# Performance work log

Measured on AMD Instinct MI355X. Metric: run time of the kernel, lower is better.

Reference implementation:

```python
import jax, jax.numpy as jnp
import numpy as np

N_NODES = 100000
N_EDGES = 1600000
IN_CH = 128
HID = 64
BN_EPS = 1e-5


def setup_inputs() -> dict:
    key = jax.random.key(0)
    ks = jax.random.split(key, 16)
    x = jax.random.normal(ks[0], (N_NODES, IN_CH), dtype=jnp.float32)
    edge_index = jax.random.randint(ks[1], (2, N_EDGES), 0, N_NODES, dtype=jnp.int32)
    edge_weight = jax.random.uniform(ks[2], (N_EDGES,), dtype=jnp.float32)
    # GCNConv layer params (weight [in, out], bias [out])
    W1 = jax.random.normal(ks[3], (IN_CH, HID), dtype=jnp.float32) / np.sqrt(IN_CH)
    b1 = jnp.zeros((HID,), jnp.float32)
    W2 = jax.random.normal(ks[4], (HID, HID), dtype=jnp.float32) / np.sqrt(HID)
    b2 = jnp.zeros((HID,), jnp.float32)
    # BatchNorm affine params
    g1 = jnp.ones((HID,), jnp.float32)
    beta1 = jnp.zeros((HID,), jnp.float32)
    g2 = jnp.ones((HID,), jnp.float32)
    beta2 = jnp.zeros((HID,), jnp.float32)
    # input projection for residual (in_channels != hidden_dim)
    pW = jax.random.normal(ks[5], (IN_CH, HID), dtype=jnp.float32) / np.sqrt(IN_CH)
    pb = jnp.zeros((HID,), jnp.float32)
    return {"x": x, "edge_index": edge_index, "edge_weight": edge_weight,
            "W1": W1, "b1": b1, "g1": g1, "beta1": beta1,
            "W2": W2, "b2": b2, "g2": g2, "beta2": beta2,
            "pW": pW, "pb": pb}


def _gcn_norm(edge_index, edge_weight, num_nodes):
    # add self-loops with weight 1, symmetric normalization (PyG gcn_norm)
    loop = jnp.arange(num_nodes, dtype=edge_index.dtype)
    row = jnp.concatenate([edge_index[0], loop])   # source
    col = jnp.concatenate([edge_index[1], loop])   # target
    w = jnp.concatenate([edge_weight, jnp.ones((num_nodes,), edge_weight.dtype)])
    deg = jax.ops.segment_sum(w, col, num_segments=num_nodes)  # weighted in-degree
    dis = jnp.where(deg > 0, jax.lax.rsqrt(jnp.where(deg > 0, deg, 1.0)), 0.0)
    norm = dis[row] * w * dis[col]  # [E+N]
    return row, col, norm


def _conv(h, W, b, row, col, norm, num_nodes):
    hw = h @ W                                      # [N, out]
    msg = hw[row] * norm[:, None]                   # gather + scale, [E+N, out]
    return jax.ops.segment_sum(msg, col, num_segments=num_nodes) + b


def _bn(h, g, beta):
    mu = jnp.mean(h, axis=0)
    var = jnp.var(h, axis=0)
    return g * (h - mu) * jax.lax.rsqrt(var + BN_EPS) + beta


def reference(x, edge_index, edge_weight, W1, b1, g1, beta1, W2, b2, g2, beta2, pW, pb):
    n = x.shape[0]
    row, col, norm = _gcn_norm(edge_index, edge_weight, n)
    residual = x @ pW + pb                          # input_proj residual
    # layer 1: conv -> BN -> ReLU -> (dropout=identity) -> + residual
    h = jax.nn.relu(_bn(_conv(x, W1, b1, row, col, norm, n), g1, beta1)) + residual
    # layer 2: conv -> BN -> ReLU -> + h_in
    h_in = h
    h = jax.nn.relu(_bn(_conv(h, W2, b2, row, col, norm, n), g2, beta2)) + h_in
    return h
```

## Files before the change

kernel.cpp:

```cpp
#include <hip/hip_runtime.h>

static constexpr float BN_EPS = 1e-5f;
typedef unsigned int uint;
typedef unsigned short ushort;
typedef __attribute__((ext_vector_type(8))) short bf16x8;
typedef __attribute__((ext_vector_type(4))) float f32x4;

__device__ __forceinline__ void fatomic_add(float* p, float v) {
  unsafeAtomicAdd(p, v);
}

__device__ __forceinline__ ushort f2bf(float f) {
  uint u = __float_as_uint(f);
  u += 0x7fffu + ((u >> 16) & 1u);
  return (ushort)(u >> 16);
}

__device__ __forceinline__ float4 bf4_decode(uint2 r) {
  return make_float4(__uint_as_float(r.x << 16), __uint_as_float(r.x & 0xffff0000u),
                     __uint_as_float(r.y << 16), __uint_as_float(r.y & 0xffff0000u));
}

__global__ void k_hist(const int* __restrict__ col, int* __restrict__ cnt,
                       int* __restrict__ rank, int e) {
  int i = blockIdx.x * 256 + threadIdx.x;
  if (i < e) rank[i] = atomicAdd(&cnt[col[i]], 1);
}

__global__ __launch_bounds__(256) void k_scan_part(const int* __restrict__ cnt,
                                                   int* __restrict__ bsum, int n) {
  __shared__ int sm[256];
  int t = threadIdx.x;
  int base = blockIdx.x * 1024 + t * 4;
  int s = 0;
#pragma unroll
  for (int j = 0; j < 4; j++) {
    int i = base + j;
    if (i < n) s += cnt[i];
  }
  sm[t] = s;
  __syncthreads();
  for (int off = 128; off > 0; off >>= 1) {
    if (t < off) sm[t] += sm[t + off];
    __syncthreads();
  }
  if (t == 0) bsum[blockIdx.x] = sm[0];
}

__global__ __launch_bounds__(1024) void k_scan_mid(int* __restrict__ bsum, int nb) {
  __shared__ int sm[1024];
  int t = threadIdx.x;
  int v = (t < nb) ? bsum[t] : 0;
  sm[t] = v;
  __syncthreads();
  for (int off = 1; off < 1024; off <<= 1) {
    int o = (t >= off) ? sm[t - off] : 0;
    __syncthreads();
    sm[t] += o;
    __syncthreads();
  }
  if (t < nb) bsum[t] = sm[t] - v;
}

__global__ __launch_bounds__(256) void k_scan_apply(const int* __restrict__ cnt,
                                                    int* __restrict__ ptr,
                                                    const int* __restrict__ bsum,
                                                    int n, int e) {
  __shared__ int sm[256];
  int t = threadIdx.x;
  int base = blockIdx.x * 1024 + t * 4;
  int v[4];
  int s = 0;
#pragma unroll
  for (int j = 0; j < 4; j++) {
    int i = base + j;
    v[j] = (i < n) ? cnt[i] : 0;
    s += v[j];
  }
  sm[t] = s;
  __syncthreads();
  for (int off = 1; off < 256; off <<= 1) {
    int o = (t >= off) ? sm[t - off] : 0;
    __syncthreads();
    sm[t] += o;
    __syncthreads();
  }
  int run = bsum[blockIdx.x] + sm[t] - s;
#pragma unroll
  for (int j = 0; j < 4; j++) {
    int i = base + j;
    if (i < n) {
      ptr[i] = run;
      run += v[j];
    }
  }
  if (blockIdx.x == 0 && t == 0) ptr[n] = e;
}

__global__ void k_fillcsr(const int* __restrict__ row, const int* __restrict__ col,
                          const float* __restrict__ ew, const int* __restrict__ ptr,
                          const int* __restrict__ rank, int2* __restrict__ spair, int e) {
  int i = blockIdx.x * 256 + threadIdx.x;
  if (i >= e) return;
  int p = ptr[col[i]] + rank[i];
  spair[p] = make_int2(row[i], __float_as_int(ew[i]));
}

__global__ void k_degdis(const int* __restrict__ ptr, const int2* __restrict__ spair,
                         float* __restrict__ dis, int n) {
  int v = blockIdx.x * 256 + threadIdx.x;
  if (v >= n) return;
  int b = ptr[v], en = ptr[v + 1];
  float s = 1.0f;
  for (int j = b; j < en; j++) s += __int_as_float(spair[j].y);
  dis[v] = rsqrtf(s);
}

__global__ void k_scale(int2* __restrict__ spair, const float* __restrict__ dis, int e) {
  int i = blockIdx.x * 256 + threadIdx.x;
  if (i >= e) return;
  int2 m = spair[i];
  spair[i] = make_int2(m.x, __float_as_int(__int_as_float(m.y) * dis[m.x]));
}

__global__ __launch_bounds__(256) void k_agg(
    const int* __restrict__ ptr, const int2* __restrict__ spair,
    const float* __restrict__ dis, const ushort* __restrict__ hwb,
    float* __restrict__ agg, float* __restrict__ stats, int n) {
  int lane = threadIdx.x & 63;
  int grp = lane >> 4;
  int li = lane & 15;
  int wid = blockIdx.x * 4 + (threadIdx.x >> 6);
  int nw = gridDim.x * 4;
  float st_s[4] = {0.f, 0.f, 0.f, 0.f};
  float st_q[4] = {0.f, 0.f, 0.f, 0.f};

  for (int vb = wid * 4; vb < n; vb += nw * 4) {
    int v = vb + grp;
    bool on = v < n;
    float4 acc = make_float4(0.f, 0.f, 0.f, 0.f);
    float d = 0.f;
    int beg = 0, end = 0;
    if (on) {
      beg = ptr[v];
      end = ptr[v + 1];
      d = dis[v];
      uint2 rs = *(const uint2*)(hwb + (size_t)v * 64 + li * 4);
      float4 f = bf4_decode(rs);
      acc = make_float4(d * f.x, d * f.y, d * f.z, d * f.w);
    }
    if (on && beg < end) {
      const int4* sp = (const int4*)spair;
      int jc = beg & ~3;
      int h = jc >> 1;
      int nch = (end - jc + 3) >> 2;

      float wA[4], wB[4], wC_[4];
      uint2 gA[4], gB[4], gC_[4];
      int4 mN0, mN1;

      {
        int4 p0 = sp[h], p1 = sp[h + 1];
        int rr[4] = {p0.x, p0.z, p1.x, p1.z};
        int wi[4] = {p0.y, p0.w, p1.y, p1.w};
#pragma unroll
        for (int k = 0; k < 4; k++) {
          int idx = jc + k;
          bool okk = (idx >= beg) && (idx < end);
          int r = okk ? rr[k] : v;
          wA[k] = okk ? __int_as_float(wi[k]) : 0.f;
          gA[k] = *(const uint2*)(hwb + (size_t)r * 64 + li * 4);
        }
      }
      if (nch > 1) {
        int4 p0 = sp[h + 2], p1 = sp[h + 3];
        int rr[4] = {p0.x, p0.z, p1.x, p1.z};
        int wi[4] = {p0.y, p0.w, p1.y, p1.w};
#pragma unroll
        for (int k = 0; k < 4; k++) {
          bool okk = (jc + 4 + k) < end;
          int r = okk ? rr[k] : v;
          wB[k] = okk ? __int_as_float(wi[k]) : 0.f;
          gB[k] = *(const uint2*)(hwb + (size_t)r * 64 + li * 4);
        }
      }
      if (nch > 2) {
        int4 p0 = sp[h + 4], p1 = sp[h + 5];
        int rr[4] = {p0.x, p0.z, p1.x, p1.z};
        int wi[4] = {p0.y, p0.w, p1.y, p1.w};
#pragma unroll
        for (int k = 0; k < 4; k++) {
          bool okk = (jc + 8 + k) < end;
          int r = okk ? rr[k] : v;
          wC_[k] = okk ? __int_as_float(wi[k]) : 0.f;
          gC_[k] = *(const uint2*)(hwb + (size_t)r * 64 + li * 4);
        }
      }
      if (nch > 3) { mN0 = sp[h + 6]; mN1 = sp[h + 7]; }

      for (int c = 0; c < nch; c++) {
        float wD[4];
        uint2 gD[4];
        if (c + 3 < nch) {
          int jn = jc + 12;
          int rr[4] = {mN0.x, mN0.z, mN1.x, mN1.z};
          int wi[4] = {mN0.y, mN0.w, mN1.y, mN1.w};
#pragma unroll
          for (int k = 0; k < 4; k++) {
            bool okk = (jn + k) < end;
            int r = okk ? rr[k] : v;
            wD[k] = okk ? __int_as_float(wi[k]) : 0.f;
            gD[k] = *(const uint2*)(hwb + (size_t)r * 64 + li * 4);
          }
        }
        if (c + 4 < nch) {
          mN0 = sp[h + 2 * (c + 4)];
          mN1 = sp[h + 2 * (c + 4) + 1];
        }
#pragma unroll
        for (int k = 0; k < 4; k++) {
          float4 f = bf4_decode(gA[k]);
          acc.x = fmaf(wA[k], f.x, acc.x);
          acc.y = fmaf(wA[k], f.y, acc.y);
          acc.z = fmaf(wA[k], f.z, acc.z);
          acc.w = fmaf(wA[k], f.w, acc.w);
        }
#pragma unroll
        for (int k = 0; k < 4; k++) {
          gA[k] = gB[k]; wA[k] = wB[k];
          gB[k] = gC_[k]; wB[k] = wC_[k];
        }
        if (c + 3 < nch) {
#pragma unroll
          for (int k = 0; k < 4; k++) { gC_[k] = gD[k]; wC_[k] = wD[k]; }
        }
        jc += 4;
      }
    }
    if (on) {
      acc.x *= d; acc.y *= d; acc.z *= d; acc.w *= d;
      *(float4*)(agg + (size_t)v * 64 + li * 4) = acc;
      st_s[0] += acc.x; st_s[1] += acc.y; st_s[2] += acc.z; st_s[3] += acc.w;
      st_q[0] = fmaf(acc.x, acc.x, st_q[0]);
      st_q[1] = fmaf(acc.y, acc.y, st_q[1]);
      st_q[2] = fmaf(acc.z, acc.z, st_q[2]);
      st_q[3] = fmaf(acc.w, acc.w, st_q[3]);
    }
  }

#pragma unroll
  for (int j = 0; j < 4; j++) {
    st_s[j] += __shfl_xor(st_s[j], 16);
    st_s[j] += __shfl_xor(st_s[j], 32);
    st_q[j] += __shfl_xor(st_q[j], 16);
    st_q[j] += __shfl_xor(st_q[j], 32);
  }
  __shared__ float rs[4][64];
  __shared__ float rq[4][64];
  int wv = threadIdx.x >> 6;
  if (grp == 0) {
#pragma unroll
    for (int j = 0; j < 4; j++) {
      rs[wv][li * 4 + j] = st_s[j];
      rq[wv][li * 4 + j] = st_q[j];
    }
  }
  __syncthreads();
  if (threadIdx.x < 64) {
    int c = threadIdx.x;
    float s = rs[0][c] + rs[1][c] + rs[2][c] + rs[3][c];
    float q = rq[0][c] + rq[1][c] + rq[2][c] + rq[3][c];
    fatomic_add(&stats[c], s);
    fatomic_add(&stats[64 + c], q);
  }
}

__global__ __launch_bounds__(256) void k_gemm1m(
    const float* __restrict__ x, const float* __restrict__ W1,
    const float* __restrict__ pW, const float* __restrict__ pb,
    ushort* __restrict__ ob, float* __restrict__ of, int n) {
  __shared__ ushort wT[128 * 128];
  int tid = threadIdx.x;
  for (int idx = tid; idx < 128 * 64; idx += 256) {
    int c = idx >> 6;
    int kp = idx & 63;
    const float* src = (c < 64) ? (W1 + c) : (pW + (c - 64));
    float f0 = src[(size_t)(2 * kp) * 64];
    float f1 = src[(size_t)(2 * kp + 1) * 64];
    uint pk = (uint)f2bf(f0) | ((uint)f2bf(f1) << 16);
    int byte = c * 256 + kp * 4;
    byte ^= ((c & 7) << 4);
    *(uint*)((char*)wT + byte) = pk;
  }
  __syncthreads();

  int lane = tid & 63;
  int wv = tid >> 6;
  int lr = lane & 15;
  int lk = lane >> 4;
  int rowBase = blockIdx.x * 128 + wv * 32;

  f32x4 acc[2][8];
#pragma unroll
  for (int i = 0; i < 2; i++)
#pragma unroll
    for (int j = 0; j < 8; j++) acc[i][j] = (f32x4){0.f, 0.f, 0.f, 0.f};

  int r0 = rowBase + lr;
  int r1 = rowBase + 16 + lr;
  bool ok0 = r0 < n, ok1 = r1 < n;
  int swz = (lr & 7) << 4;

#pragma unroll
  for (int ks = 0; ks < 4; ks++) {
    int k0 = ks * 32 + lk * 8;
    bf16x8 a0 = (bf16x8)(short)0, a1 = (bf16x8)(short)0;
    if (ok0) {
      const float4* xp = (const float4*)(x + (size_t)r0 * 128 + k0);
      float4 v0 = xp[0], v1 = xp[1];
      a0[0] = (short)f2bf(v0.x); a0[1] = (short)f2bf(v0.y);
      a0[2] = (short)f2bf(v0.z); a0[3] = (short)f2bf(v0.w);
      a0[4] = (short)f2bf(v1.x); a0[5] = (short)f2bf(v1.y);
      a0[6] = (short)f2bf(v1.z); a0[7] = (short)f2bf(v1.w);
    }
    if (ok1) {
      const float4* xp = (const float4*)(x + (size_t)r1 * 128 + k0);
      float4 v0 = xp[0], v1 = xp[1];
      a1[0] = (short)f2bf(v0.x); a1[1] = (short)f2bf(v0.y);
      a1[2] = (short)f2bf(v0.z); a1[3] = (short)f2bf(v0.w);
      a1[4] = (short)f2bf(v1.x); a1[5] = (short)f2bf(v1.y);
      a1[6] = (short)f2bf(v1.z); a1[7] = (short)f2bf(v1.w);
    }
#pragma unroll
    for (int ct = 0; ct < 8; ct++) {
      int byte = ((ct * 16 + lr) * 128 + k0) * 2;
      byte ^= swz;
      bf16x8 b = *(const bf16x8*)((const char*)wT + byte);
      acc[0][ct] = __builtin_amdgcn_mfma_f32_16x16x32_bf16(a0, b, acc[0][ct], 0, 0, 0);
      acc[1][ct] = __builtin_amdgcn_mfma_f32_16x16x32_bf16(a1, b, acc[1][ct], 0, 0, 0);
    }
  }

  float bias[4];
#pragma unroll
  for (int q = 0; q < 4; q++) bias[q] = pb[q * 16 + lr];

#pragma unroll
  for (int rt = 0; rt < 2; rt++) {
#pragma unroll
    for (int e = 0; e < 4; e++) {
      int r = rowBase + rt * 16 + lk * 4 + e;
      if (r >= n) continue;
#pragma unroll
      for (int ct = 0; ct < 4; ct++)
        ob[(size_t)r * 64 + ct * 16 + lr] = f2bf(acc[rt][ct][e]);
#pragma unroll
      for (int ct = 4; ct < 8; ct++)
        of[(size_t)r * 64 + (ct - 4) * 16 + lr] = acc[rt][ct][e] + bias[ct - 4];
    }
  }
}

__global__ __launch_bounds__(256) void k_gemm2m(
    const float* __restrict__ h, const float* __restrict__ W2,
    ushort* __restrict__ ob, int n) {
  __shared__ ushort wT[64 * 64];
  int tid = threadIdx.x;
  for (int idx = tid; idx < 64 * 32; idx += 256) {
    int c = idx >> 5;
    int kp = idx & 31;
    float f0 = W2[(size_t)(2 * kp) * 64 + c];
    float f1 = W2[(size_t)(2 * kp + 1) * 64 + c];
    uint pk = (uint)f2bf(f0) | ((uint)f2bf(f1) << 16);
    int byte = c * 128 + kp * 4;
    byte ^= ((c & 7) << 4);
    *(uint*)((char*)wT + byte) = pk;
  }
  __syncthreads();

  int lane = tid & 63;
  int wv = tid >> 6;
  int lr = lane & 15;
  int lk = lane >> 4;
  int rowBase = blockIdx.x * 128 + wv * 32;

  f32x4 acc[2][4];
#pragma unroll
  for (int i = 0; i < 2; i++)
#pragma unroll
    for (int j = 0; j < 4; j++) acc[i][j] = (f32x4){0.f, 0.f, 0.f, 0.f};

  int r0 = rowBase + lr;
  int r1 = rowBase + 16 + lr;
  bool ok0 = r0 < n, ok1 = r1 < n;
  int swz = (lr & 7) << 4;

#pragma unroll
  for (int ks = 0; ks < 2; ks++) {
    int k0 = ks * 32 + lk * 8;
    bf16x8 a0 = (bf16x8)(short)0, a1 = (bf16x8)(short)0;
    if (ok0) {
      const float4* xp = (const float4*)(h + (size_t)r0 * 64 + k0);
      float4 v0 = xp[0], v1 = xp[1];
      a0[0] = (short)f2bf(v0.x); a0[1] = (short)f2bf(v0.y);
      a0[2] = (short)f2bf(v0.z); a0[3] = (short)f2bf(v0.w);
      a0[4] = (short)f2bf(v1.x); a0[5] = (short)f2bf(v1.y);
      a0[6] = (short)f2bf(v1.z); a0[7] = (short)f2bf(v1.w);
    }
    if (ok1) {
      const float4* xp = (const float4*)(h + (size_t)r1 * 64 + k0);
      float4 v0 = xp[0], v1 = xp[1];
      a1[0] = (short)f2bf(v0.x); a1[1] = (short)f2bf(v0.y);
      a1[2] = (short)f2bf(v0.z); a1[3] = (short)f2bf(v0.w);
      a1[4] = (short)f2bf(v1.x); a1[5] = (short)f2bf(v1.y);
      a1[6] = (short)f2bf(v1.z); a1[7] = (short)f2bf(v1.w);
    }
#pragma unroll
    for (int ct = 0; ct < 4; ct++) {
      int byte = ((ct * 16 + lr) * 64 + k0) * 2;
      byte ^= swz;
      bf16x8 b = *(const bf16x8*)((const char*)wT + byte);
      acc[0][ct] = __builtin_amdgcn_mfma_f32_16x16x32_bf16(a0, b, acc[0][ct], 0, 0, 0);
      acc[1][ct] = __builtin_amdgcn_mfma_f32_16x16x32_bf16(a1, b, acc[1][ct], 0, 0, 0);
    }
  }

#pragma unroll
  for (int rt = 0; rt < 2; rt++) {
#pragma unroll
    for (int e = 0; e < 4; e++) {
      int r = rowBase + rt * 16 + lk * 4 + e;
      if (r >= n) continue;
#pragma unroll
      for (int ct = 0; ct < 4; ct++)
        ob[(size_t)r * 64 + ct * 16 + lr] = f2bf(acc[rt][ct][e]);
    }
  }
}

__global__ __launch_bounds__(256) void k_bnrelu(
    const float* __restrict__ agg, const float* __restrict__ res,
    const float* __restrict__ stats, const float* __restrict__ g,
    const float* __restrict__ beta, float* __restrict__ out, int n) {
  int idx = blockIdx.x * 256 + threadIdx.x;
  if (idx >= n * 16) return;
  int c4 = (idx & 15) * 4;
  float invN = 1.0f / (float)n;
  float4 a = ((const float4*)agg)[idx];
  float4 rr = ((const float4*)res)[idx];
  float av[4] = {a.x, a.y, a.z, a.w};
  float rv[4] = {rr.x, rr.y, rr.z, rr.w};
  float vo[4];
#pragma unroll
  for (int j = 0; j < 4; j++) {
    int c = c4 + j;
    float mu = stats[c] * invN;
    float var = stats[64 + c] * invN - mu * mu;
    float sc = g[c] * rsqrtf(var + BN_EPS);
    float v = (av[j] - mu) * sc + beta[c];
    vo[j] = fmaxf(v, 0.0f) + rv[j];
  }
  ((float4*)out)[idx] = make_float4(vo[0], vo[1], vo[2], vo[3]);
}

extern "C" void kernel_launch(void* const* d_in, const int* in_sizes, int n_in,
                              void* d_out, int out_size, void* d_ws, size_t ws_size,
                              hipStream_t stream) {
  const float* x = (const float*)d_in[0];
  const int* ei = (const int*)d_in[1];
  const float* ew = (const float*)d_in[2];
  const float* W1 = (const float*)d_in[3];
  const float* g1 = (const float*)d_in[5];
  const float* be1 = (const float*)d_in[6];
  const float* W2 = (const float*)d_in[7];
  const float* g2 = (const float*)d_in[9];
  const float* be2 = (const float*)d_in[10];
  const float* pW = (const float*)d_in[11];
  const float* pb = (const float*)d_in[12];

  int n = in_sizes[0] / 128;
  int e = in_sizes[1] / 2;
  const int* row = ei;
  const int* col = ei + e;

  float* ws = (float*)d_ws;
  float* dis = ws;
  int* ptr = (int*)(dis + n);
  int* cnt = ptr + n + 4;
  int* rank = cnt + n;
  int* bsum = rank + e;
  int2* spair = (int2*)(bsum + 1024);
  ushort* hwb = (ushort*)(spair + e + 32);
  float* bufR = (float*)(hwb + (size_t)n * 64);
  float* bufB = bufR + (size_t)n * 64;
  float* bufA = bufB + (size_t)n * 64;
  float* stats = bufA + (size_t)n * 64;

  float* out = (float*)d_out;

  int nb_n = (n + 255) / 256;
  int nb_e = (e + 255) / 256;
  int nb_b = (n * 16 + 255) / 256;
  int nb_sc = (n + 1023) / 1024;
  int nb_g = (n + 127) / 128;

  hipMemsetAsync(cnt, 0, n * sizeof(int), stream);
  k_hist<<<nb_e, 256, 0, stream>>>(col, cnt, rank, e);
  k_scan_part<<<nb_sc, 256, 0, stream>>>(cnt, bsum, n);
  k_scan_mid<<<1, 1024, 0, stream>>>(bsum, nb_sc);
  k_scan_apply<<<nb_sc, 256, 0, stream>>>(cnt, ptr, bsum, n, e);
  k_fillcsr<<<nb_e, 256, 0, stream>>>(row, col, ew, ptr, rank, spair, e);
  k_degdis<<<nb_n, 256, 0, stream>>>(ptr, spair, dis, n);
  k_scale<<<nb_e, 256, 0, stream>>>(spair, dis, e);

  k_gemm1m<<<nb_g, 256, 0, stream>>>(x, W1, pW, pb, hwb, bufR, n);
  hipMemsetAsync(stats, 0, 128 * sizeof(float), stream);
  k_agg<<<2048, 256, 0, stream>>>(ptr, spair, dis, hwb, bufB, stats, n);
  k_bnrelu<<<nb_b, 256, 0, stream>>>(bufB, bufR, stats, g1, be1, bufA, n);

  k_gemm2m<<<nb_g, 256, 0, stream>>>(bufA, W2, hwb, n);
  hipMemsetAsync(stats, 0, 128 * sizeof(float), stream);
  k_agg<<<2048, 256, 0, stream>>>(ptr, spair, dis, hwb, bufB, stats, n);
  k_bnrelu<<<nb_b, 256, 0, stream>>>(bufB, bufA, stats, g2, be2, out, n);
}
```

Baseline: 409.4 us.

## Aggregate contiguous node ranges per 16-lane group with a continuous edge pipeline

```diff
diff --git a/kernel.cpp b/kernel.cpp
--- a/kernel.cpp
+++ b/kernel.cpp
@@ -126,34 +126,60 @@
 __global__ __launch_bounds__(256) void k_agg(
     const int* __restrict__ ptr, const int2* __restrict__ spair,
     const float* __restrict__ dis, const ushort* __restrict__ hwb,
-    float* __restrict__ agg, float* __restrict__ stats, int n) {
-  int lane = threadIdx.x & 63;
-  int grp = lane >> 4;
+    float* __restrict__ agg, float* __restrict__ stats, int n, int npg) {
+  int tid = threadIdx.x;
+  int lane = tid & 63;
   int li = lane & 15;
-  int wid = blockIdx.x * 4 + (threadIdx.x >> 6);
-  int nw = gridDim.x * 4;
+  int gbase = lane & 48;
+  int gidx = (blockIdx.x * 256 + tid) >> 4;
   float st_s[4] = {0.f, 0.f, 0.f, 0.f};
   float st_q[4] = {0.f, 0.f, 0.f, 0.f};
 
-  for (int vb = wid * 4; vb < n; vb += nw * 4) {
-    int v = vb + grp;
-    bool on = v < n;
+  int v0 = gidx * npg;
+  if (v0 < n) {
+    int v1 = min(v0 + npg, n);
+    int tmax = v1 - v0;
+    int pv = ptr[min(v0 + li, n)];
+    float dvr = dis[min(v0 + li, n - 1)];
+    int begR = __shfl(pv, gbase);
+    int jend = __shfl(pv, gbase + tmax);
+
+    int v = v0, t = 0;
+    float d = __shfl(dvr, gbase);
+    int e_cur = __shfl(pv, gbase + 1);
+    uint2 self_cur = *(const uint2*)(hwb + (size_t)v0 * 64 + li * 4);
+    uint2 self_nxt = *(const uint2*)(hwb + (size_t)min(v0 + 1, n - 1) * 64 + li * 4);
+    int vself = v0 + 2;
     float4 acc = make_float4(0.f, 0.f, 0.f, 0.f);
-    float d = 0.f;
-    int beg = 0, end = 0;
-    if (on) {
-      beg = ptr[v];
-      end = ptr[v + 1];
-      d = dis[v];
-      uint2 rs = *(const uint2*)(hwb + (size_t)v * 64 + li * 4);
-      float4 f = bf4_decode(rs);
-      acc = make_float4(d * f.x, d * f.y, d * f.z, d * f.w);
-    }
-    if (on && beg < end) {
+
+#define FINALIZE_NODE()                                                        \
+  {                                                                            \
+    float4 sf = bf4_decode(self_cur);                                          \
+    float4 o;                                                                  \
+    o.x = d * fmaf(d, sf.x, acc.x);                                            \
+    o.y = d * fmaf(d, sf.y, acc.y);                                            \
+    o.z = d * fmaf(d, sf.z, acc.z);                                            \
+    o.w = d * fmaf(d, sf.w, acc.w);                                            \
+    *(float4*)(agg + (size_t)v * 64 + li * 4) = o;                             \
+    st_s[0] += o.x; st_s[1] += o.y; st_s[2] += o.z; st_s[3] += o.w;            \
+    st_q[0] = fmaf(o.x, o.x, st_q[0]);                                         \
+    st_q[1] = fmaf(o.y, o.y, st_q[1]);                                         \
+    st_q[2] = fmaf(o.z, o.z, st_q[2]);                                         \
+    st_q[3] = fmaf(o.w, o.w, st_q[3]);                                         \
+    acc = make_float4(0.f, 0.f, 0.f, 0.f);                                     \
+    self_cur = self_nxt;                                                       \
+    self_nxt = *(const uint2*)(hwb + (size_t)min(vself, n - 1) * 64 + li * 4); \
+    vself++;                                                                   \
+    v++; t++;                                                                  \
+    d = __shfl(dvr, gbase + min(t, 15));                                       \
+    e_cur = __shfl(pv, gbase + min(t + 1, 15));                                \
+  }
+
+    if (begR < jend) {
       const int4* sp = (const int4*)spair;
-      int jc = beg & ~3;
+      int jc = begR & ~3;
       int h = jc >> 1;
-      int nch = (end - jc + 3) >> 2;
+      int nch = (jend - jc + 3) >> 2;
 
       float wA[4], wB[4], wC_[4];
       uint2 gA[4], gB[4], gC_[4];
@@ -165,9 +191,9 @@
         int wi[4] = {p0.y, p0.w, p1.y, p1.w};
 #pragma unroll
         for (int k = 0; k < 4; k++) {
-          int idx = jc + k;
-          bool okk = (idx >= beg) && (idx < end);
-          int r = okk ? rr[k] : v;
+          int j = jc + k;
+          bool okk = (j >= begR) && (j < jend);
+          int r = okk ? rr[k] : v0;
           wA[k] = okk ? __int_as_float(wi[k]) : 0.f;
           gA[k] = *(const uint2*)(hwb + (size_t)r * 64 + li * 4);
         }
@@ -178,8 +204,8 @@
         int wi[4] = {p0.y, p0.w, p1.y, p1.w};
 #pragma unroll
         for (int k = 0; k < 4; k++) {
-          bool okk = (jc + 4 + k) < end;
-          int r = okk ? rr[k] : v;
+          bool okk = (jc + 4 + k) < jend;
+          int r = okk ? rr[k] : v0;
           wB[k] = okk ? __int_as_float(wi[k]) : 0.f;
           gB[k] = *(const uint2*)(hwb + (size_t)r * 64 + li * 4);
         }
@@ -190,8 +216,8 @@
         int wi[4] = {p0.y, p0.w, p1.y, p1.w};
 #pragma unroll
         for (int k = 0; k < 4; k++) {
-          bool okk = (jc + 8 + k) < end;
-          int r = okk ? rr[k] : v;
+          bool okk = (jc + 8 + k) < jend;
+          int r = okk ? rr[k] : v0;
           wC_[k] = okk ? __int_as_float(wi[k]) : 0.f;
           gC_[k] = *(const uint2*)(hwb + (size_t)r * 64 + li * 4);
         }
@@ -207,8 +233,8 @@
           int wi[4] = {mN0.y, mN0.w, mN1.y, mN1.w};
 #pragma unroll
           for (int k = 0; k < 4; k++) {
-            bool okk = (jn + k) < end;
-            int r = okk ? rr[k] : v;
+            bool okk = (jn + k) < jend;
+            int r = okk ? rr[k] : v0;
             wD[k] = okk ? __int_as_float(wi[k]) : 0.f;
             gD[k] = *(const uint2*)(hwb + (size_t)r * 64 + li * 4);
           }
@@ -219,6 +245,8 @@
         }
 #pragma unroll
         for (int k = 0; k < 4; k++) {
+          int j = jc + k;
+          while (j >= e_cur && v < v1) FINALIZE_NODE();
           float4 f = bf4_decode(gA[k]);
           acc.x = fmaf(wA[k], f.x, acc.x);
           acc.y = fmaf(wA[k], f.y, acc.y);
@@ -237,15 +265,8 @@
         jc += 4;
       }
     }
-    if (on) {
-      acc.x *= d; acc.y *= d; acc.z *= d; acc.w *= d;
-      *(float4*)(agg + (size_t)v * 64 + li * 4) = acc;
-      st_s[0] += acc.x; st_s[1] += acc.y; st_s[2] += acc.z; st_s[3] += acc.w;
-      st_q[0] = fmaf(acc.x, acc.x, st_q[0]);
-      st_q[1] = fmaf(acc.y, acc.y, st_q[1]);
-      st_q[2] = fmaf(acc.z, acc.z, st_q[2]);
-      st_q[3] = fmaf(acc.w, acc.w, st_q[3]);
-    }
+    while (v < v1) FINALIZE_NODE();
+#undef FINALIZE_NODE
   }
 
 #pragma unroll
@@ -257,8 +278,8 @@
   }
   __shared__ float rs[4][64];
   __shared__ float rq[4][64];
-  int wv = threadIdx.x >> 6;
-  if (grp == 0) {
+  int wv = tid >> 6;
+  if (gbase == 0) {
 #pragma unroll
     for (int j = 0; j < 4; j++) {
       rs[wv][li * 4 + j] = st_s[j];
@@ -266,8 +287,8 @@
     }
   }
   __syncthreads();
-  if (threadIdx.x < 64) {
-    int c = threadIdx.x;
+  if (tid < 64) {
+    int c = tid;
     float s = rs[0][c] + rs[1][c] + rs[2][c] + rs[3][c];
     float q = rq[0][c] + rq[1][c] + rq[2][c] + rq[3][c];
     fatomic_add(&stats[c], s);
@@ -504,6 +525,10 @@
   int nb_sc = (n + 1023) / 1024;
   int nb_g = (n + 127) / 128;
 
+  constexpr int AGG_BLOCKS = 1024;
+  int ngroups = AGG_BLOCKS * 16;
+  int npg = (n + ngroups - 1) / ngroups;
+
   hipMemsetAsync(cnt, 0, n * sizeof(int), stream);
   k_hist<<<nb_e, 256, 0, stream>>>(col, cnt, rank, e);
   k_scan_part<<<nb_sc, 256, 0, stream>>>(cnt, bsum, n);
@@ -515,11 +540,11 @@
 
   k_gemm1m<<<nb_g, 256, 0, stream>>>(x, W1, pW, pb, hwb, bufR, n);
   hipMemsetAsync(stats, 0, 128 * sizeof(float), stream);
-  k_agg<<<2048, 256, 0, stream>>>(ptr, spair, dis, hwb, bufB, stats, n);
+  k_agg<<<AGG_BLOCKS, 256, 0, stream>>>(ptr, spair, dis, hwb, bufB, stats, n, npg);
   k_bnrelu<<<nb_b, 256, 0, stream>>>(bufB, bufR, stats, g1, be1, bufA, n);
 
   k_gemm2m<<<nb_g, 256, 0, stream>>>(bufA, W2, hwb, n);
   hipMemsetAsync(stats, 0, 128 * sizeof(float), stream);
-  k_agg<<<2048, 256, 0, stream>>>(ptr, spair, dis, hwb, bufB, stats, n);
+  k_agg<<<AGG_BLOCKS, 256, 0, stream>>>(ptr, spair, dis, hwb, bufB, stats, n, npg);
   k_bnrelu<<<nb_b, 256, 0, stream>>>(bufB, bufA, stats, g2, be2, out, n);
 }
```

Result: faster. 383.6 us (-6.3%).
